# Kernel optimization log

Measured on AMD Instinct MI355X. Metric: run time of the kernel, lower is better.

Reference implementation:

```python
import jax, jax.numpy as jnp
import numpy as np

N_NODES = 100000
N_EDGES = 1600000
IN_F, HID_F, OUT_F = 64, 64, 16


def setup_inputs() -> dict:
    key = jax.random.key(0)
    k_x, k_e, k_w1, k_w2 = jax.random.split(key, 4)
    x = jax.random.normal(k_x, (N_NODES, IN_F), dtype=jnp.float32)
    edge_index = jax.random.randint(k_e, (2, N_EDGES), 0, N_NODES, dtype=jnp.int64)
    # Glorot-ish init for the GCNConv linear weights; bias zeros (PyG default)
    W1 = jax.random.normal(k_w1, (IN_F, HID_F), dtype=jnp.float32) / np.sqrt(IN_F)
    b1 = jnp.zeros((HID_F,), dtype=jnp.float32)
    W2 = jax.random.normal(k_w2, (HID_F, OUT_F), dtype=jnp.float32) / np.sqrt(HID_F)
    b2 = jnp.zeros((OUT_F,), dtype=jnp.float32)
    return {"x": x, "edge_index": edge_index, "W1": W1, "b1": b1, "W2": W2, "b2": b2}


def reference(x, edge_index, W1, b1, W2, b2):
    N = x.shape[0]
    # GCNConv: add self-loops, symmetric normalization D^-1/2 A D^-1/2
    loop = jnp.arange(N, dtype=edge_index.dtype)
    src = jnp.concatenate([edge_index[0], loop])  # [E+N]
    dst = jnp.concatenate([edge_index[1], loop])  # [E+N]
    deg = jax.ops.segment_sum(jnp.ones_like(dst, dtype=x.dtype), dst, num_segments=N)
    dis = jax.lax.rsqrt(deg)  # deg >= 1 due to self-loops
    norm = dis[src] * dis[dst]  # [E+N]

    def gcn_conv(h, W, b):
        h = h @ W                                   # [N, d_out]
        msg = h[src] * norm[:, None]                # gather + scale  [E+N, d_out]
        agg = jax.ops.segment_sum(msg, dst, num_segments=N)  # scatter-add
        return agg + b

    h = jax.nn.relu(gcn_conv(x, W1, b1))
    h = gcn_conv(h, W2, b2)
    return jax.nn.log_softmax(h, axis=1)
```

## Files before the change

kernel.cpp:

```cpp
#include <hip/hip_runtime.h>
#include <hip/hip_bf16.h>
#include <hip/hip_fp16.h>


#define F1 64
#define F2 16
#define NBKT 256
#define BSH 512
#define NSB 256
#define SBD 1024
#define STG 9216

typedef _Float16 f16x8 __attribute__((ext_vector_type(8)));
typedef _Float16 f16x4 __attribute__((ext_vector_type(4)));
typedef float f32x2 __attribute__((ext_vector_type(2)));
typedef float f32x4 __attribute__((ext_vector_type(4)));
typedef float f32x8 __attribute__((ext_vector_type(8)));

__device__ inline f32x8 shfl_xor_f32x8(f32x8 v, int off) {
  f32x8 r;
#pragma unroll
  for (int k = 0; k < 8; ++k) r[k] = __shfl_xor(v[k], off);
  return r;
}
__device__ inline f32x4 shfl_xor_f32x4(f32x4 v, int off) {
  f32x4 r;
#pragma unroll
  for (int k = 0; k < 4; ++k) r[k] = __shfl_xor(v[k], off);
  return r;
}

__device__ inline void acc_fp8x8(f32x8& a, uint2 v) {
  f32x2 p0 = __builtin_amdgcn_cvt_pk_f32_fp8((int)v.x, false);
  f32x2 p1 = __builtin_amdgcn_cvt_pk_f32_fp8((int)v.x, true);
  f32x2 p2 = __builtin_amdgcn_cvt_pk_f32_fp8((int)v.y, false);
  f32x2 p3 = __builtin_amdgcn_cvt_pk_f32_fp8((int)v.y, true);
  a[0] += p0[0]; a[1] += p0[1]; a[2] += p1[0]; a[3] += p1[1];
  a[4] += p2[0]; a[5] += p2[1]; a[6] += p3[0]; a[7] += p3[1];
}

__global__ void k_scatterL(const int* __restrict__ src, const int* __restrict__ dst,
                           int* __restrict__ tmp, int* __restrict__ segstart,
                           int E, int nb, int chunk,
                           const float* __restrict__ W1, const float* __restrict__ W2,
                           const float* __restrict__ b1,
                           __half* __restrict__ W1T, __half* __restrict__ W2Tp,
                           float* __restrict__ b1p) {
  int t = threadIdx.x, sb = blockIdx.x;
  if (sb == NSB) {
    for (int i = t; i < 64 * 64; i += SBD) {
      int n = i >> 6, k = i & 63;
      W1T[i] = __float2half(W1[k * 64 + n]);
    }
    for (int i = t; i < 16 * 64; i += SBD) {
      int j = i >> 6, p = i & 63;
      int fp = 16 * (p & 3) + (p >> 2);
      W2Tp[i] = __float2half(W2[fp * 16 + j]);
    }
    if (t < 64) b1p[t] = b1[16 * (t & 3) + (t >> 2)];
    return;
  }
  __shared__ int h[NBKT];
  __shared__ int cur[NBKT];
  __shared__ int sc[NBKT];
  int beg = sb * chunk, end = min(beg + chunk, E);
  for (int i = t; i < NBKT; i += SBD) h[i] = 0;
  __syncthreads();
  int e;
  for (e = beg + t * 4; e + 4 <= end; e += 4 * SBD) {
    int4 d4 = *(const int4*)(dst + e);
    atomicAdd(&h[d4.x >> 9], 1);
    atomicAdd(&h[d4.y >> 9], 1);
    atomicAdd(&h[d4.z >> 9], 1);
    atomicAdd(&h[d4.w >> 9], 1);
  }
  for (; e < end; ++e) atomicAdd(&h[dst[e] >> 9], 1);
  __syncthreads();
  if (t < NBKT) sc[t] = h[t];
  __syncthreads();
  for (int off = 1; off < NBKT; off <<= 1) {
    int a = (t < NBKT && t >= off) ? sc[t - off] : 0;
    __syncthreads();
    if (t < NBKT) sc[t] += a;
    __syncthreads();
  }
  if (t < NBKT) cur[t] = (t == 0) ? 0 : sc[t - 1];
  __syncthreads();
  for (int i = t; i < nb; i += SBD) segstart[sb * (nb + 1) + i] = beg + cur[i];
  if (t == 0) segstart[sb * (nb + 1) + nb] = end;
  __syncthreads();
  for (e = beg + t * 4; e + 4 <= end; e += 4 * SBD) {
    int4 d4 = *(const int4*)(dst + e);
    int4 s4 = *(const int4*)(src + e);
    int b, off;
    b = d4.x >> 9; off = atomicAdd(&cur[b], 1); tmp[beg + off] = (s4.x << 9) | (d4.x & 511);
    b = d4.y >> 9; off = atomicAdd(&cur[b], 1); tmp[beg + off] = (s4.y << 9) | (d4.y & 511);
    b = d4.z >> 9; off = atomicAdd(&cur[b], 1); tmp[beg + off] = (s4.z << 9) | (d4.z & 511);
    b = d4.w >> 9; off = atomicAdd(&cur[b], 1); tmp[beg + off] = (s4.w << 9) | (d4.w & 511);
  }
  for (; e < end; ++e) {
    int d = dst[e];
    int b = d >> 9;
    int off = atomicAdd(&cur[b], 1);
    tmp[beg + off] = (src[e] << 9) | (d & 511);
  }
}

__global__ void k_csr(const int* __restrict__ tmp, const int* __restrict__ segstart,
                      int* __restrict__ csr, int* __restrict__ rowptr,
                      float* __restrict__ dis, int N, int nb, int chunk) {
  __shared__ int stage[STG];
  __shared__ int sc[BSH];
  __shared__ int cnt[BSH];
  __shared__ int lofs[BSH];
  __shared__ int s_beg;
  int b = blockIdx.x, t = threadIdx.x;
  int s0 = 0, len = 0;
  if (t < NSB) {
    s0 = segstart[t * (nb + 1) + b];
    len = segstart[t * (nb + 1) + b + 1] - s0;
  }
  sc[t] = (t < NSB) ? (s0 - t * chunk) : 0;
  __syncthreads();
  for (int off = BSH / 2; off > 0; off >>= 1) {
    if (t < off) sc[t] += sc[t + off];
    __syncthreads();
  }
  if (t == 0) s_beg = sc[0];
  __syncthreads();
  int beg = s_beg;
  sc[t] = (t < NSB) ? len : 0;
  __syncthreads();
  for (int off = 1; off < NSB; off <<= 1) {
    int a = (t < NSB && t >= off) ? sc[t - off] : 0;
    __syncthreads();
    if (t < NSB) sc[t] += a;
    __syncthreads();
  }
  int total = sc[NSB - 1];
  int my0 = (t == 0) ? 0 : ((t < NSB) ? sc[t - 1] : 0);
  if (t < NSB) {
    int i = 0;
    for (; i + 4 <= len; i += 4) {
      int v0 = tmp[s0 + i], v1 = tmp[s0 + i + 1], v2 = tmp[s0 + i + 2], v3 = tmp[s0 + i + 3];
      stage[my0 + i] = v0; stage[my0 + i + 1] = v1;
      stage[my0 + i + 2] = v2; stage[my0 + i + 3] = v3;
    }
    for (; i < len; ++i) stage[my0 + i] = tmp[s0 + i];
  }
  cnt[t] = 0;
  __syncthreads();
  for (int i = t; i < total; i += BSH) atomicAdd(&cnt[stage[i] & (BSH - 1)], 1);
  __syncthreads();
  sc[t] = cnt[t];
  __syncthreads();
  for (int off = 1; off < BSH; off <<= 1) {
    int a = (t >= off) ? sc[t - off] : 0;
    __syncthreads();
    sc[t] += a;
    __syncthreads();
  }
  int excl = (t == 0) ? 0 : sc[t - 1];
  lofs[t] = excl;
  int n = b * BSH + t;
  if (n <= N) rowptr[n] = beg + excl;
  if (n < N) dis[n] = rsqrtf((float)(cnt[t] + 1));
  cnt[t] = 0;
  __syncthreads();
  for (int i = t; i < total; i += BSH) {
    int p = stage[i];
    int l = p & (BSH - 1);
    int off = atomicAdd(&cnt[l], 1);
    csr[beg + lofs[l] + off] = p >> 9;
  }
}

__global__ void k_gemm1(const float* __restrict__ x, const __half* __restrict__ W1T,
                        const float* __restrict__ dis, unsigned char* __restrict__ out,
                        int N) {
  int t = threadIdx.x;
  int wv = t >> 6, lane = t & 63;
  int m = lane & 15, q = lane >> 4;
  int row0 = blockIdx.x * 64 + wv * 16;
  int arow = min(row0 + m, N - 1);
  const _Float16* wt = (const _Float16*)W1T;
  f16x8 bf[4][2];
#pragma unroll
  for (int c = 0; c < 4; ++c)
#pragma unroll
    for (int kt = 0; kt < 2; ++kt)
      bf[c][kt] = *(const f16x8*)&wt[(c * 16 + m) * 64 + kt * 32 + q * 8];
  f16x8 a[2];
#pragma unroll
  for (int kt = 0; kt < 2; ++kt) {
    const float4* xp = (const float4*)(x + (size_t)arow * 64 + kt * 32 + q * 8);
    float4 u = xp[0], v = xp[1];
    a[kt][0] = (_Float16)u.x; a[kt][1] = (_Float16)u.y;
    a[kt][2] = (_Float16)u.z; a[kt][3] = (_Float16)u.w;
    a[kt][4] = (_Float16)v.x; a[kt][5] = (_Float16)v.y;
    a[kt][6] = (_Float16)v.z; a[kt][7] = (_Float16)v.w;
  }
  f32x4 acc[4] = {};
#pragma unroll
  for (int kt = 0; kt < 2; ++kt)
#pragma unroll
    for (int c = 0; c < 4; ++c)
      acc[c] = __builtin_amdgcn_mfma_f32_16x16x32_f16(a[kt], bf[c][kt], acc[c], 0, 0, 0);
#pragma unroll
  for (int r = 0; r < 4; ++r) {
    int n = row0 + q * 4 + r;
    if (n < N) {
      float dn = dis[n];
      int d = __builtin_amdgcn_cvt_pk_fp8_f32(acc[0][r] * dn, acc[1][r] * dn, 0, false);
      d = __builtin_amdgcn_cvt_pk_fp8_f32(acc[2][r] * dn, acc[3][r] * dn, d, true);
      *(unsigned int*)(out + (size_t)n * 64 + m * 4) = (unsigned)d;
    }
  }
}

__global__ void k_agg1f(const unsigned char* __restrict__ h, const float* __restrict__ dis,
                        const int* __restrict__ rowptr, const int* __restrict__ csr,
                        const float* __restrict__ b1p, const __half* __restrict__ W2Tp,
                        __half* __restrict__ h2, int N) {
  int gt = blockIdx.x * blockDim.x + threadIdx.x;
  int w = gt >> 6;
  int lane = gt & 63;
  int half = lane >> 5;
  int sub = (lane >> 3) & 3;
  int fl = lane & 7;
  int n = w * 2 + half;
  if (n >= N) return;
  float dn = dis[n];
  float4 bu = *(const float4*)(b1p + fl * 8);
  float4 bv = *(const float4*)(b1p + fl * 8 + 4);
  const _Float16* wt = (const _Float16*)W2Tp;
  f16x8 wj[4];
#pragma unroll
  for (int i = 0; i < 4; ++i)
    wj[i] = *(const f16x8*)&wt[(sub * 4 + i) * 64 + fl * 8];
  f32x8 acc0 = {}, acc1 = {};
  if (sub == 0)
    acc_fp8x8(acc0, *(const uint2*)&h[(size_t)n * 64 + fl * 8]);
  int beg = rowptr[n], end = rowptr[n + 1];
  int e = beg + sub;
  int sA = (e < end) ? csr[e] : -1;
  int sB = (e + 4 < end) ? csr[e + 4] : -1;
  while (sB >= 0) {
    int e2 = e + 8;
    int sC = (e2 < end) ? csr[e2] : -1;
    int sD = (e2 + 4 < end) ? csr[e2 + 4] : -1;
    uint2 v0 = *(const uint2*)&h[(size_t)sA * 64 + fl * 8];
    uint2 v1 = *(const uint2*)&h[(size_t)sB * 64 + fl * 8];
    acc_fp8x8(acc0, v0);
    acc_fp8x8(acc1, v1);
    sA = sC; sB = sD; e = e2;
  }
  if (sA >= 0)
    acc_fp8x8(acc0, *(const uint2*)&h[(size_t)sA * 64 + fl * 8]);
  f32x8 acc = acc0 + acc1;
  acc += shfl_xor_f32x8(acc, 8);
  acc += shfl_xor_f32x8(acc, 16);
  float bb[8] = {bu.x, bu.y, bu.z, bu.w, bv.x, bv.y, bv.z, bv.w};
  float hr[8];
#pragma unroll
  for (int k = 0; k < 8; ++k)
    hr[k] = fmaxf(fmaf(dn, acc[k], bb[k]), 0.f);
  float p[4];
#pragma unroll
  for (int i = 0; i < 4; ++i) {
    float s = 0.f;
#pragma unroll
    for (int k = 0; k < 8; ++k) s = fmaf(hr[k], (float)wj[i][k], s);
    s += __shfl_xor(s, 1);
    s += __shfl_xor(s, 2);
    s += __shfl_xor(s, 4);
    p[i] = s;
  }
  if (fl == 0) {
    f16x4 o;
#pragma unroll
    for (int i = 0; i < 4; ++i) o[i] = (_Float16)(p[i] * dn);
    *(f16x4*)((_Float16*)h2 + (size_t)n * 16 + sub * 4) = o;
  }
}

__global__ void k_agg2(const __half* __restrict__ h2, const float* __restrict__ dis,
                       const int* __restrict__ rowptr, const int* __restrict__ csr,
                       const float* __restrict__ b2, float* __restrict__ out, int N) {
  int gt = blockIdx.x * blockDim.x + threadIdx.x;
  int w = gt >> 6;
  int lane = gt & 63;
  int half = lane >> 5;
  int sub = (lane >> 2) & 7;
  int fl = lane & 3;
  int n = w * 2 + half;
  if (n >= N) return;
  const _Float16* hp = (const _Float16*)h2;
  f32x4 acc0 = {}, acc1 = {};
  if (sub == 0)
    acc0 = __builtin_convertvector(*(const f16x4*)&hp[(size_t)n * 16 + fl * 4], f32x4);
  int beg = rowptr[n], end = rowptr[n + 1];
  int e = beg + sub;
  int sA = (e < end) ? csr[e] : -1;
  int sB = (e + 8 < end) ? csr[e + 8] : -1;
  while (sB >= 0) {
    int e2 = e + 16;
    int sC = (e2 < end) ? csr[e2] : -1;
    int sD = (e2 + 8 < end) ? csr[e2 + 8] : -1;
    f16x4 v0 = *(const f16x4*)&hp[(size_t)sA * 16 + fl * 4];
    f16x4 v1 = *(const f16x4*)&hp[(size_t)sB * 16 + fl * 4];
    acc0 += __builtin_convertvector(v0, f32x4);
    acc1 += __builtin_convertvector(v1, f32x4);
    sA = sC; sB = sD; e = e2;
  }
  if (sA >= 0)
    acc0 += __builtin_convertvector(*(const f16x4*)&hp[(size_t)sA * 16 + fl * 4], f32x4);
  f32x4 acc = acc0 + acc1;
  acc += shfl_xor_f32x4(acc, 4);
  acc += shfl_xor_f32x4(acc, 8);
  acc += shfl_xor_f32x4(acc, 16);
  if (sub == 0) {
    float dn = dis[n];
    float4 bb = *(const float4*)(b2 + fl * 4);
    float v0 = fmaf(dn, acc[0], bb.x);
    float v1 = fmaf(dn, acc[1], bb.y);
    float v2 = fmaf(dn, acc[2], bb.z);
    float v3 = fmaf(dn, acc[3], bb.w);
    float m = fmaxf(fmaxf(v0, v1), fmaxf(v2, v3));
    m = fmaxf(m, __shfl_xor(m, 1));
    m = fmaxf(m, __shfl_xor(m, 2));
    float s2 = __expf(v0 - m) + __expf(v1 - m) + __expf(v2 - m) + __expf(v3 - m);
    s2 += __shfl_xor(s2, 1);
    s2 += __shfl_xor(s2, 2);
    float ls = m + __logf(s2);
    float4 o = {v0 - ls, v1 - ls, v2 - ls, v3 - ls};
    *(float4*)(out + (size_t)n * 16 + fl * 4) = o;
  }
}

extern "C" void kernel_launch(void* const* d_in, const int* in_sizes, int n_in,
                              void* d_out, int out_size, void* d_ws, size_t ws_size,
                              hipStream_t stream) {
  const float* x = (const float*)d_in[0];
  const int* ei = (const int*)d_in[1];
  const float* W1 = (const float*)d_in[2];
  const float* b1 = (const float*)d_in[3];
  const float* W2 = (const float*)d_in[4];
  const float* b2 = (const float*)d_in[5];
  float* out = (float*)d_out;

  int N = in_sizes[0] / F1;
  int E = in_sizes[1] / 2;
  const int* src = ei;
  const int* dst = ei + E;
  int nb = (N + BSH - 1) >> 9;
  int chunk = ((E + NSB - 1) / NSB + 3) & ~3;

  char* ws = (char*)d_ws;
  size_t o_w1t = 0;
  size_t o_w2t = o_w1t + 64 * 64 * 2;
  size_t o_b1p = (o_w2t + 16 * 64 * 2 + 255) & ~(size_t)255;
  size_t o_seg = (o_b1p + 64 * 4 + 255) & ~(size_t)255;
  size_t o_dis = (o_seg + (size_t)NSB * (nb + 1) * 4 + 255) & ~(size_t)255;
  size_t o_rowp = (o_dis + (size_t)N * 4 + 255) & ~(size_t)255;
  size_t o_tmp = (o_rowp + (size_t)(N + 1) * 4 + 255) & ~(size_t)255;
  size_t o_csr = (o_tmp + (size_t)NSB * chunk * 4 + 255) & ~(size_t)255;
  size_t o_h1 = (o_csr + (size_t)E * 4 + 255) & ~(size_t)255;
  size_t o_h2 = (o_h1 + (size_t)N * 64 + 255) & ~(size_t)255;

  __half* W1T = (__half*)(ws + o_w1t);
  __half* W2Tp = (__half*)(ws + o_w2t);
  float* b1p = (float*)(ws + o_b1p);
  int* segst = (int*)(ws + o_seg);
  float* dis = (float*)(ws + o_dis);
  int* rowptr = (int*)(ws + o_rowp);
  int* tmp = (int*)(ws + o_tmp);
  int* csr = (int*)(ws + o_csr);
  unsigned char* h1 = (unsigned char*)(ws + o_h1);
  __half* h2 = (__half*)(ws + o_h2);

  k_scatterL<<<NSB + 1, SBD, 0, stream>>>(src, dst, tmp, segst, E, nb, chunk,
                                          W1, W2, b1, W1T, W2Tp, b1p);
  k_csr<<<nb, BSH, 0, stream>>>(tmp, segst, csr, rowptr, dis, N, nb, chunk);

  int gb = (N + 63) / 64;
  k_gemm1<<<gb, 256, 0, stream>>>(x, W1T, dis, h1, N);
  int aw = (N + 1) / 2;
  k_agg1f<<<((size_t)aw * 64 + 255) / 256, 256, 0, stream>>>(h1, dis, rowptr, csr, b1p, W2Tp, h2, N);
  k_agg2<<<((size_t)aw * 64 + 255) / 256, 256, 0, stream>>>(h2, dis, rowptr, csr, b2, out, N);
}
```

Before: 181.1 us.

## Replace two-pass bucketed CSR build with global-atomic degree count and fill

Replaces the shared-memory bucket sort (per-block histogram, segment offsets, and a per-bucket staging/counting-sort kernel) with a global atomic degree histogram, a wave-scan allocation of row segments through an atomic counter, and an atomic-cursor fill of the CSR. Rows are no longer contiguous in node order, so the aggregation kernels read separate begin/end arrays. The intent is fewer passes and less shared-memory staging, at the cost of many scattered global atomics and a less local CSR write pattern. The fp8 accumulator is also reshaped into f32x2 pieces.

```diff
diff --git a/kernel.cpp b/kernel.cpp
--- a/kernel.cpp
+++ b/kernel.cpp
@@ -5,11 +5,8 @@
 
 #define F1 64
 #define F2 16
-#define NBKT 256
-#define BSH 512
-#define NSB 256
+#define NPB 256
 #define SBD 1024
-#define STG 9216
 
 typedef _Float16 f16x8 __attribute__((ext_vector_type(8)));
 typedef _Float16 f16x4 __attribute__((ext_vector_type(4)));
@@ -30,24 +27,20 @@
   return r;
 }
 
-__device__ inline void acc_fp8x8(f32x8& a, uint2 v) {
-  f32x2 p0 = __builtin_amdgcn_cvt_pk_f32_fp8((int)v.x, false);
-  f32x2 p1 = __builtin_amdgcn_cvt_pk_f32_fp8((int)v.x, true);
-  f32x2 p2 = __builtin_amdgcn_cvt_pk_f32_fp8((int)v.y, false);
-  f32x2 p3 = __builtin_amdgcn_cvt_pk_f32_fp8((int)v.y, true);
-  a[0] += p0[0]; a[1] += p0[1]; a[2] += p1[0]; a[3] += p1[1];
-  a[4] += p2[0]; a[5] += p2[1]; a[6] += p3[0]; a[7] += p3[1];
-}
-
-__global__ void k_scatterL(const int* __restrict__ src, const int* __restrict__ dst,
-                           int* __restrict__ tmp, int* __restrict__ segstart,
-                           int E, int nb, int chunk,
-                           const float* __restrict__ W1, const float* __restrict__ W2,
-                           const float* __restrict__ b1,
-                           __half* __restrict__ W1T, __half* __restrict__ W2Tp,
-                           float* __restrict__ b1p) {
+__device__ inline void acc_fp8x8(f32x2* a, uint2 v) {
+  a[0] += __builtin_amdgcn_cvt_pk_f32_fp8((int)v.x, false);
+  a[1] += __builtin_amdgcn_cvt_pk_f32_fp8((int)v.x, true);
+  a[2] += __builtin_amdgcn_cvt_pk_f32_fp8((int)v.y, false);
+  a[3] += __builtin_amdgcn_cvt_pk_f32_fp8((int)v.y, true);
+}
+
+__global__ void k_pre(const int* __restrict__ dst, int* __restrict__ deg, int E,
+                      const float* __restrict__ W1, const float* __restrict__ W2,
+                      const float* __restrict__ b1,
+                      __half* __restrict__ W1T, __half* __restrict__ W2Tp,
+                      float* __restrict__ b1p) {
   int t = threadIdx.x, sb = blockIdx.x;
-  if (sb == NSB) {
+  if (sb == NPB) {
     for (int i = t; i < 64 * 64; i += SBD) {
       int n = i >> 6, k = i & 63;
       W1T[i] = __float2half(W1[k * 64 + n]);
@@ -60,118 +53,65 @@
     if (t < 64) b1p[t] = b1[16 * (t & 3) + (t >> 2)];
     return;
   }
-  __shared__ int h[NBKT];
-  __shared__ int cur[NBKT];
-  __shared__ int sc[NBKT];
-  int beg = sb * chunk, end = min(beg + chunk, E);
-  for (int i = t; i < NBKT; i += SBD) h[i] = 0;
-  __syncthreads();
-  int e;
-  for (e = beg + t * 4; e + 4 <= end; e += 4 * SBD) {
-    int4 d4 = *(const int4*)(dst + e);
-    atomicAdd(&h[d4.x >> 9], 1);
-    atomicAdd(&h[d4.y >> 9], 1);
-    atomicAdd(&h[d4.z >> 9], 1);
-    atomicAdd(&h[d4.w >> 9], 1);
-  }
-  for (; e < end; ++e) atomicAdd(&h[dst[e] >> 9], 1);
-  __syncthreads();
-  if (t < NBKT) sc[t] = h[t];
-  __syncthreads();
-  for (int off = 1; off < NBKT; off <<= 1) {
-    int a = (t < NBKT && t >= off) ? sc[t - off] : 0;
-    __syncthreads();
-    if (t < NBKT) sc[t] += a;
-    __syncthreads();
-  }
-  if (t < NBKT) cur[t] = (t == 0) ? 0 : sc[t - 1];
-  __syncthreads();
-  for (int i = t; i < nb; i += SBD) segstart[sb * (nb + 1) + i] = beg + cur[i];
-  if (t == 0) segstart[sb * (nb + 1) + nb] = end;
-  __syncthreads();
-  for (e = beg + t * 4; e + 4 <= end; e += 4 * SBD) {
-    int4 d4 = *(const int4*)(dst + e);
-    int4 s4 = *(const int4*)(src + e);
-    int b, off;
-    b = d4.x >> 9; off = atomicAdd(&cur[b], 1); tmp[beg + off] = (s4.x << 9) | (d4.x & 511);
-    b = d4.y >> 9; off = atomicAdd(&cur[b], 1); tmp[beg + off] = (s4.y << 9) | (d4.y & 511);
-    b = d4.z >> 9; off = atomicAdd(&cur[b], 1); tmp[beg + off] = (s4.z << 9) | (d4.z & 511);
-    b = d4.w >> 9; off = atomicAdd(&cur[b], 1); tmp[beg + off] = (s4.w << 9) | (d4.w & 511);
-  }
-  for (; e < end; ++e) {
-    int d = dst[e];
-    int b = d >> 9;
-    int off = atomicAdd(&cur[b], 1);
-    tmp[beg + off] = (src[e] << 9) | (d & 511);
-  }
-}
-
-__global__ void k_csr(const int* __restrict__ tmp, const int* __restrict__ segstart,
-                      int* __restrict__ csr, int* __restrict__ rowptr,
-                      float* __restrict__ dis, int N, int nb, int chunk) {
-  __shared__ int stage[STG];
-  __shared__ int sc[BSH];
-  __shared__ int cnt[BSH];
-  __shared__ int lofs[BSH];
-  __shared__ int s_beg;
-  int b = blockIdx.x, t = threadIdx.x;
-  int s0 = 0, len = 0;
-  if (t < NSB) {
-    s0 = segstart[t * (nb + 1) + b];
-    len = segstart[t * (nb + 1) + b + 1] - s0;
-  }
-  sc[t] = (t < NSB) ? (s0 - t * chunk) : 0;
-  __syncthreads();
-  for (int off = BSH / 2; off > 0; off >>= 1) {
-    if (t < off) sc[t] += sc[t + off];
-    __syncthreads();
-  }
-  if (t == 0) s_beg = sc[0];
-  __syncthreads();
-  int beg = s_beg;
-  sc[t] = (t < NSB) ? len : 0;
-  __syncthreads();
-  for (int off = 1; off < NSB; off <<= 1) {
-    int a = (t < NSB && t >= off) ? sc[t - off] : 0;
-    __syncthreads();
-    if (t < NSB) sc[t] += a;
-    __syncthreads();
-  }
-  int total = sc[NSB - 1];
-  int my0 = (t == 0) ? 0 : ((t < NSB) ? sc[t - 1] : 0);
-  if (t < NSB) {
-    int i = 0;
-    for (; i + 4 <= len; i += 4) {
-      int v0 = tmp[s0 + i], v1 = tmp[s0 + i + 1], v2 = tmp[s0 + i + 2], v3 = tmp[s0 + i + 3];
-      stage[my0 + i] = v0; stage[my0 + i + 1] = v1;
-      stage[my0 + i + 2] = v2; stage[my0 + i + 3] = v3;
-    }
-    for (; i < len; ++i) stage[my0 + i] = tmp[s0 + i];
-  }
-  cnt[t] = 0;
-  __syncthreads();
-  for (int i = t; i < total; i += BSH) atomicAdd(&cnt[stage[i] & (BSH - 1)], 1);
-  __syncthreads();
-  sc[t] = cnt[t];
-  __syncthreads();
-  for (int off = 1; off < BSH; off <<= 1) {
-    int a = (t >= off) ? sc[t - off] : 0;
-    __syncthreads();
-    sc[t] += a;
-    __syncthreads();
-  }
-  int excl = (t == 0) ? 0 : sc[t - 1];
-  lofs[t] = excl;
-  int n = b * BSH + t;
-  if (n <= N) rowptr[n] = beg + excl;
-  if (n < N) dis[n] = rsqrtf((float)(cnt[t] + 1));
-  cnt[t] = 0;
-  __syncthreads();
-  for (int i = t; i < total; i += BSH) {
-    int p = stage[i];
-    int l = p & (BSH - 1);
-    int off = atomicAdd(&cnt[l], 1);
-    csr[beg + lofs[l] + off] = p >> 9;
+  int e4 = E >> 2;
+  int stride = NPB * SBD;
+  const int4* d4p = (const int4*)dst;
+  for (int i = sb * SBD + t; i < e4; i += stride) {
+    int4 d4 = d4p[i];
+    atomicAdd(&deg[d4.x], 1);
+    atomicAdd(&deg[d4.y], 1);
+    atomicAdd(&deg[d4.z], 1);
+    atomicAdd(&deg[d4.w], 1);
+  }
+  int tid = sb * SBD + t;
+  if (tid < (E & 3)) atomicAdd(&deg[dst[(E & ~3) + tid]], 1);
+}
+
+__global__ void k_alloc(const int* __restrict__ deg, int* __restrict__ ctr,
+                        int* __restrict__ rowbeg, int* __restrict__ rowcur,
+                        float* __restrict__ dis, int N) {
+  int n = blockIdx.x * blockDim.x + threadIdx.x;
+  int lane = threadIdx.x & 63;
+  int d = (n < N) ? deg[n] : 0;
+  int v = d;
+#pragma unroll
+  for (int off = 1; off < 64; off <<= 1) {
+    int u = __shfl_up(v, off);
+    if (lane >= off) v += u;
+  }
+  int tot = __shfl(v, 63);
+  int wbase = 0;
+  if (lane == 0) wbase = atomicAdd(ctr, tot);
+  wbase = __shfl(wbase, 0);
+  if (n < N) {
+    int b0 = wbase + v - d;
+    rowbeg[n] = b0;
+    rowcur[n] = b0;
+    dis[n] = rsqrtf((float)(d + 1));
+  }
+}
+
+__global__ void k_fill(const int* __restrict__ src, const int* __restrict__ dst,
+                       int* __restrict__ rowcur, int* __restrict__ csr, int E) {
+  int t = threadIdx.x, sb = blockIdx.x;
+  int e4 = E >> 2;
+  int stride = NPB * SBD;
+  const int4* d4p = (const int4*)dst;
+  const int4* s4p = (const int4*)src;
+  for (int i = sb * SBD + t; i < e4; i += stride) {
+    int4 d4 = d4p[i];
+    int4 s4 = s4p[i];
+    int o;
+    o = atomicAdd(&rowcur[d4.x], 1); csr[o] = s4.x;
+    o = atomicAdd(&rowcur[d4.y], 1); csr[o] = s4.y;
+    o = atomicAdd(&rowcur[d4.z], 1); csr[o] = s4.z;
+    o = atomicAdd(&rowcur[d4.w], 1); csr[o] = s4.w;
+  }
+  int tid = sb * SBD + t;
+  if (tid < (E & 3)) {
+    int e = (E & ~3) + tid;
+    int o = atomicAdd(&rowcur[dst[e]], 1);
+    csr[o] = src[e];
   }
 }
 
@@ -219,7 +159,8 @@
 }
 
 __global__ void k_agg1f(const unsigned char* __restrict__ h, const float* __restrict__ dis,
-                        const int* __restrict__ rowptr, const int* __restrict__ csr,
+                        const int* __restrict__ rowbeg, const int* __restrict__ rowcur,
+                        const int* __restrict__ csr,
                         const float* __restrict__ b1p, const __half* __restrict__ W2Tp,
                         __half* __restrict__ h2, int N) {
   int gt = blockIdx.x * blockDim.x + threadIdx.x;
@@ -238,10 +179,10 @@
 #pragma unroll
   for (int i = 0; i < 4; ++i)
     wj[i] = *(const f16x8*)&wt[(sub * 4 + i) * 64 + fl * 8];
-  f32x8 acc0 = {}, acc1 = {};
+  f32x2 a0[4] = {}, a1[4] = {};
   if (sub == 0)
-    acc_fp8x8(acc0, *(const uint2*)&h[(size_t)n * 64 + fl * 8]);
-  int beg = rowptr[n], end = rowptr[n + 1];
+    acc_fp8x8(a0, *(const uint2*)&h[(size_t)n * 64 + fl * 8]);
+  int beg = rowbeg[n], end = rowcur[n];
   int e = beg + sub;
   int sA = (e < end) ? csr[e] : -1;
   int sB = (e + 4 < end) ? csr[e + 4] : -1;
@@ -251,13 +192,19 @@
     int sD = (e2 + 4 < end) ? csr[e2 + 4] : -1;
     uint2 v0 = *(const uint2*)&h[(size_t)sA * 64 + fl * 8];
     uint2 v1 = *(const uint2*)&h[(size_t)sB * 64 + fl * 8];
-    acc_fp8x8(acc0, v0);
-    acc_fp8x8(acc1, v1);
+    acc_fp8x8(a0, v0);
+    acc_fp8x8(a1, v1);
     sA = sC; sB = sD; e = e2;
   }
   if (sA >= 0)
-    acc_fp8x8(acc0, *(const uint2*)&h[(size_t)sA * 64 + fl * 8]);
-  f32x8 acc = acc0 + acc1;
+    acc_fp8x8(a0, *(const uint2*)&h[(size_t)sA * 64 + fl * 8]);
+  f32x8 acc;
+#pragma unroll
+  for (int k = 0; k < 4; ++k) {
+    f32x2 s = a0[k] + a1[k];
+    acc[2 * k] = s[0];
+    acc[2 * k + 1] = s[1];
+  }
   acc += shfl_xor_f32x8(acc, 8);
   acc += shfl_xor_f32x8(acc, 16);
   float bb[8] = {bu.x, bu.y, bu.z, bu.w, bv.x, bv.y, bv.z, bv.w};
@@ -285,7 +232,8 @@
 }
 
 __global__ void k_agg2(const __half* __restrict__ h2, const float* __restrict__ dis,
-                       const int* __restrict__ rowptr, const int* __restrict__ csr,
+                       const int* __restrict__ rowbeg, const int* __restrict__ rowcur,
+                       const int* __restrict__ csr,
                        const float* __restrict__ b2, float* __restrict__ out, int N) {
   int gt = blockIdx.x * blockDim.x + threadIdx.x;
   int w = gt >> 6;
@@ -299,7 +247,7 @@
   f32x4 acc0 = {}, acc1 = {};
   if (sub == 0)
     acc0 = __builtin_convertvector(*(const f16x4*)&hp[(size_t)n * 16 + fl * 4], f32x4);
-  int beg = rowptr[n], end = rowptr[n + 1];
+  int beg = rowbeg[n], end = rowcur[n];
   int e = beg + sub;
   int sA = (e < end) ? csr[e] : -1;
   int sB = (e + 8 < end) ? csr[e + 8] : -1;
@@ -353,39 +301,38 @@
   int E = in_sizes[1] / 2;
   const int* src = ei;
   const int* dst = ei + E;
-  int nb = (N + BSH - 1) >> 9;
-  int chunk = ((E + NSB - 1) / NSB + 3) & ~3;
 
   char* ws = (char*)d_ws;
   size_t o_w1t = 0;
   size_t o_w2t = o_w1t + 64 * 64 * 2;
   size_t o_b1p = (o_w2t + 16 * 64 * 2 + 255) & ~(size_t)255;
-  size_t o_seg = (o_b1p + 64 * 4 + 255) & ~(size_t)255;
-  size_t o_dis = (o_seg + (size_t)NSB * (nb + 1) * 4 + 255) & ~(size_t)255;
-  size_t o_rowp = (o_dis + (size_t)N * 4 + 255) & ~(size_t)255;
-  size_t o_tmp = (o_rowp + (size_t)(N + 1) * 4 + 255) & ~(size_t)255;
-  size_t o_csr = (o_tmp + (size_t)NSB * chunk * 4 + 255) & ~(size_t)255;
-  size_t o_h1 = (o_csr + (size_t)E * 4 + 255) & ~(size_t)255;
-  size_t o_h2 = (o_h1 + (size_t)N * 64 + 255) & ~(size_t)255;
+  size_t o_deg = (o_b1p + 64 * 4 + 255) & ~(size_t)255;
+  size_t o_rbg = (o_deg + (size_t)(N + 64) * 4 + 255) & ~(size_t)255;
+  size_t o_rcu = (o_rbg + (size_t)N * 4 + 255) & ~(size_t)255;
+  size_t o_dis = (o_rcu + (size_t)N * 4 + 255) & ~(size_t)255;
+  size_t o_csr = (o_dis + (size_t)N * 4 + 255) & ~(size_t)255;
+  size_t o_h1  = (o_csr + (size_t)E * 4 + 255) & ~(size_t)255;
+  size_t o_h2  = (o_h1 + (size_t)N * 64 + 255) & ~(size_t)255;
 
   __half* W1T = (__half*)(ws + o_w1t);
   __half* W2Tp = (__half*)(ws + o_w2t);
   float* b1p = (float*)(ws + o_b1p);
-  int* segst = (int*)(ws + o_seg);
+  int* deg = (int*)(ws + o_deg);
+  int* ctr = deg + N;
+  int* rowbeg = (int*)(ws + o_rbg);
+  int* rowcur = (int*)(ws + o_rcu);
   float* dis = (float*)(ws + o_dis);
-  int* rowptr = (int*)(ws + o_rowp);
-  int* tmp = (int*)(ws + o_tmp);
   int* csr = (int*)(ws + o_csr);
   unsigned char* h1 = (unsigned char*)(ws + o_h1);
   __half* h2 = (__half*)(ws + o_h2);
 
-  k_scatterL<<<NSB + 1, SBD, 0, stream>>>(src, dst, tmp, segst, E, nb, chunk,
-                                          W1, W2, b1, W1T, W2Tp, b1p);
-  k_csr<<<nb, BSH, 0, stream>>>(tmp, segst, csr, rowptr, dis, N, nb, chunk);
-
+  hipMemsetAsync(deg, 0, (size_t)(N + 64) * 4, stream);
+  k_pre<<<NPB + 1, SBD, 0, stream>>>(dst, deg, E, W1, W2, b1, W1T, W2Tp, b1p);
+  k_alloc<<<(N + 255) / 256, 256, 0, stream>>>(deg, ctr, rowbeg, rowcur, dis, N);
+  k_fill<<<NPB, SBD, 0, stream>>>(src, dst, rowcur, csr, E);
   int gb = (N + 63) / 64;
   k_gemm1<<<gb, 256, 0, stream>>>(x, W1T, dis, h1, N);
   int aw = (N + 1) / 2;
-  k_agg1f<<<((size_t)aw * 64 + 255) / 256, 256, 0, stream>>>(h1, dis, rowptr, csr, b1p, W2Tp, h2, N);
-  k_agg2<<<((size_t)aw * 64 + 255) / 256, 256, 0, stream>>>(h2, dis, rowptr, csr, b2, out, N);
-}
+  k_agg1f<<<((size_t)aw * 64 + 255) / 256, 256, 0, stream>>>(h1, dis, rowbeg, rowcur, csr, b1p, W2Tp, h2, N);
+  k_agg2<<<((size_t)aw * 64 + 255) / 256, 256, 0, stream>>>(h2, dis, rowbeg, rowcur, csr, b2, out, N);
+}
```

Measured after the change: 329.4 us. 82.0% more time.

## Fuse layer-1 GEMM into edge scatter kernel by moving source normalization to aggregation

Applied to the files above, without the earlier changes.

The layer-1 GEMM no longer scales its output by dis[n], so it no longer depends on the degree computation. Its blocks now run inside the edge bucketing kernel as extra blocks and overlap with the scatter. The source-side dis factor is applied in the layer-1 aggregation with a per-edge dis gather and packed FMAs. The weight preparation moves to a separate single-block kernel, and the scatter stage is reshaped to 512 blocks of 256 threads. The cost is an extra random dis load per edge in aggregation, plus fp8 quantization of unscaled values, which changes rounding.

```diff
diff --git a/kernel.cpp b/kernel.cpp
--- a/kernel.cpp
+++ b/kernel.cpp
@@ -7,8 +7,8 @@
 #define F2 16
 #define NBKT 256
 #define BSH 512
-#define NSB 256
-#define SBD 1024
+#define NSB 512
+#define SBD 256
 #define STG 9216
 
 typedef _Float16 f16x8 __attribute__((ext_vector_type(8)));
@@ -30,41 +30,82 @@
   return r;
 }
 
-__device__ inline void acc_fp8x8(f32x8& a, uint2 v) {
-  f32x2 p0 = __builtin_amdgcn_cvt_pk_f32_fp8((int)v.x, false);
-  f32x2 p1 = __builtin_amdgcn_cvt_pk_f32_fp8((int)v.x, true);
-  f32x2 p2 = __builtin_amdgcn_cvt_pk_f32_fp8((int)v.y, false);
-  f32x2 p3 = __builtin_amdgcn_cvt_pk_f32_fp8((int)v.y, true);
-  a[0] += p0[0]; a[1] += p0[1]; a[2] += p1[0]; a[3] += p1[1];
-  a[4] += p2[0]; a[5] += p2[1]; a[6] += p3[0]; a[7] += p3[1];
-}
-
-__global__ void k_scatterL(const int* __restrict__ src, const int* __restrict__ dst,
-                           int* __restrict__ tmp, int* __restrict__ segstart,
-                           int E, int nb, int chunk,
-                           const float* __restrict__ W1, const float* __restrict__ W2,
-                           const float* __restrict__ b1,
-                           __half* __restrict__ W1T, __half* __restrict__ W2Tp,
-                           float* __restrict__ b1p) {
+__device__ inline void fma_fp8x8(f32x2* a, uint2 v, float s) {
+  f32x2 sv = {s, s};
+  a[0] += sv * __builtin_amdgcn_cvt_pk_f32_fp8((int)v.x, false);
+  a[1] += sv * __builtin_amdgcn_cvt_pk_f32_fp8((int)v.x, true);
+  a[2] += sv * __builtin_amdgcn_cvt_pk_f32_fp8((int)v.y, false);
+  a[3] += sv * __builtin_amdgcn_cvt_pk_f32_fp8((int)v.y, true);
+}
+
+__global__ void k_w(const float* __restrict__ W1, const float* __restrict__ W2,
+                    const float* __restrict__ b1,
+                    __half* __restrict__ W1T, __half* __restrict__ W2Tp,
+                    float* __restrict__ b1p) {
+  int t = threadIdx.x;
+  for (int i = t; i < 64 * 64; i += 256) {
+    int n = i >> 6, k = i & 63;
+    W1T[i] = __float2half(W1[k * 64 + n]);
+  }
+  for (int i = t; i < 16 * 64; i += 256) {
+    int j = i >> 6, p = i & 63;
+    int fp = 16 * (p & 3) + (p >> 2);
+    W2Tp[i] = __float2half(W2[fp * 16 + j]);
+  }
+  if (t < 64) b1p[t] = b1[16 * (t & 3) + (t >> 2)];
+}
+
+__global__ void k_sg(const int* __restrict__ src, const int* __restrict__ dst,
+                     int* __restrict__ tmp, int* __restrict__ segstart,
+                     int E, int nb, int chunk,
+                     const float* __restrict__ x, const __half* __restrict__ W1T,
+                     unsigned char* __restrict__ h1, int N) {
   int t = threadIdx.x, sb = blockIdx.x;
-  if (sb == NSB) {
-    for (int i = t; i < 64 * 64; i += SBD) {
-      int n = i >> 6, k = i & 63;
-      W1T[i] = __float2half(W1[k * 64 + n]);
+  if (sb >= NSB) {
+    int g = sb - NSB;
+    int wv = t >> 6, lane = t & 63;
+    int m = lane & 15, q = lane >> 4;
+    int row0 = g * 64 + wv * 16;
+    int arow = min(row0 + m, N - 1);
+    const _Float16* wt = (const _Float16*)W1T;
+    f16x8 bf[4][2];
+#pragma unroll
+    for (int c = 0; c < 4; ++c)
+#pragma unroll
+      for (int kt = 0; kt < 2; ++kt)
+        bf[c][kt] = *(const f16x8*)&wt[(c * 16 + m) * 64 + kt * 32 + q * 8];
+    f16x8 a[2];
+#pragma unroll
+    for (int kt = 0; kt < 2; ++kt) {
+      const float4* xp = (const float4*)(x + (size_t)arow * 64 + kt * 32 + q * 8);
+      float4 u = xp[0], v = xp[1];
+      a[kt][0] = (_Float16)u.x; a[kt][1] = (_Float16)u.y;
+      a[kt][2] = (_Float16)u.z; a[kt][3] = (_Float16)u.w;
+      a[kt][4] = (_Float16)v.x; a[kt][5] = (_Float16)v.y;
+      a[kt][6] = (_Float16)v.z; a[kt][7] = (_Float16)v.w;
     }
-    for (int i = t; i < 16 * 64; i += SBD) {
-      int j = i >> 6, p = i & 63;
-      int fp = 16 * (p & 3) + (p >> 2);
-      W2Tp[i] = __float2half(W2[fp * 16 + j]);
+    f32x4 acc[4] = {};
+#pragma unroll
+    for (int kt = 0; kt < 2; ++kt)
+#pragma unroll
+      for (int c = 0; c < 4; ++c)
+        acc[c] = __builtin_amdgcn_mfma_f32_16x16x32_f16(a[kt], bf[c][kt], acc[c], 0, 0, 0);
+#pragma unroll
+    for (int r = 0; r < 4; ++r) {
+      int n = row0 + q * 4 + r;
+      if (n < N) {
+        int d = __builtin_amdgcn_cvt_pk_fp8_f32(acc[0][r], acc[1][r], 0, false);
+        d = __builtin_amdgcn_cvt_pk_fp8_f32(acc[2][r], acc[3][r], d, true);
+        *(unsigned int*)(h1 + (size_t)n * 64 + m * 4) = (unsigned)d;
+      }
     }
-    if (t < 64) b1p[t] = b1[16 * (t & 3) + (t >> 2)];
     return;
   }
   __shared__ int h[NBKT];
   __shared__ int cur[NBKT];
   __shared__ int sc[NBKT];
   int beg = sb * chunk, end = min(beg + chunk, E);
-  for (int i = t; i < NBKT; i += SBD) h[i] = 0;
+  h[t] = 0;
   __syncthreads();
   int e;
   for (e = beg + t * 4; e + 4 <= end; e += 4 * SBD) {
@@ -76,17 +117,17 @@
   }
   for (; e < end; ++e) atomicAdd(&h[dst[e] >> 9], 1);
   __syncthreads();
-  if (t < NBKT) sc[t] = h[t];
+  sc[t] = h[t];
   __syncthreads();
   for (int off = 1; off < NBKT; off <<= 1) {
-    int a = (t < NBKT && t >= off) ? sc[t - off] : 0;
-    __syncthreads();
-    if (t < NBKT) sc[t] += a;
-    __syncthreads();
-  }
-  if (t < NBKT) cur[t] = (t == 0) ? 0 : sc[t - 1];
-  __syncthreads();
-  for (int i = t; i < nb; i += SBD) segstart[sb * (nb + 1) + i] = beg + cur[i];
+    int a = (t >= off) ? sc[t - off] : 0;
+    __syncthreads();
+    sc[t] += a;
+    __syncthreads();
+  }
+  cur[t] = (t == 0) ? 0 : sc[t - 1];
+  __syncthreads();
+  if (t < nb) segstart[sb * (nb + 1) + t] = beg + cur[t];
   if (t == 0) segstart[sb * (nb + 1) + nb] = end;
   __syncthreads();
   for (e = beg + t * 4; e + 4 <= end; e += 4 * SBD) {
@@ -115,12 +156,9 @@
   __shared__ int lofs[BSH];
   __shared__ int s_beg;
   int b = blockIdx.x, t = threadIdx.x;
-  int s0 = 0, len = 0;
-  if (t < NSB) {
-    s0 = segstart[t * (nb + 1) + b];
-    len = segstart[t * (nb + 1) + b + 1] - s0;
-  }
-  sc[t] = (t < NSB) ? (s0 - t * chunk) : 0;
+  int s0 = segstart[t * (nb + 1) + b];
+  int len = segstart[t * (nb + 1) + b + 1] - s0;
+  sc[t] = s0 - t * chunk;
   __syncthreads();
   for (int off = BSH / 2; off > 0; off >>= 1) {
     if (t < off) sc[t] += sc[t + off];
@@ -129,17 +167,17 @@
   if (t == 0) s_beg = sc[0];
   __syncthreads();
   int beg = s_beg;
-  sc[t] = (t < NSB) ? len : 0;
+  sc[t] = len;
   __syncthreads();
   for (int off = 1; off < NSB; off <<= 1) {
-    int a = (t < NSB && t >= off) ? sc[t - off] : 0;
-    __syncthreads();
-    if (t < NSB) sc[t] += a;
+    int a = (t >= off) ? sc[t - off] : 0;
+    __syncthreads();
+    sc[t] += a;
     __syncthreads();
   }
   int total = sc[NSB - 1];
-  int my0 = (t == 0) ? 0 : ((t < NSB) ? sc[t - 1] : 0);
-  if (t < NSB) {
+  int my0 = (t == 0) ? 0 : sc[t - 1];
+  {
     int i = 0;
     for (; i + 4 <= len; i += 4) {
       int v0 = tmp[s0 + i], v1 = tmp[s0 + i + 1], v2 = tmp[s0 + i + 2], v3 = tmp[s0 + i + 3];
@@ -172,49 +210,6 @@
     int l = p & (BSH - 1);
     int off = atomicAdd(&cnt[l], 1);
     csr[beg + lofs[l] + off] = p >> 9;
-  }
-}
-
-__global__ void k_gemm1(const float* __restrict__ x, const __half* __restrict__ W1T,
-                        const float* __restrict__ dis, unsigned char* __restrict__ out,
-                        int N) {
-  int t = threadIdx.x;
-  int wv = t >> 6, lane = t & 63;
-  int m = lane & 15, q = lane >> 4;
-  int row0 = blockIdx.x * 64 + wv * 16;
-  int arow = min(row0 + m, N - 1);
-  const _Float16* wt = (const _Float16*)W1T;
-  f16x8 bf[4][2];
-#pragma unroll
-  for (int c = 0; c < 4; ++c)
-#pragma unroll
-    for (int kt = 0; kt < 2; ++kt)
-      bf[c][kt] = *(const f16x8*)&wt[(c * 16 + m) * 64 + kt * 32 + q * 8];
-  f16x8 a[2];
-#pragma unroll
-  for (int kt = 0; kt < 2; ++kt) {
-    const float4* xp = (const float4*)(x + (size_t)arow * 64 + kt * 32 + q * 8);
-    float4 u = xp[0], v = xp[1];
-    a[kt][0] = (_Float16)u.x; a[kt][1] = (_Float16)u.y;
-    a[kt][2] = (_Float16)u.z; a[kt][3] = (_Float16)u.w;
-    a[kt][4] = (_Float16)v.x; a[kt][5] = (_Float16)v.y;
-    a[kt][6] = (_Float16)v.z; a[kt][7] = (_Float16)v.w;
-  }
-  f32x4 acc[4] = {};
-#pragma unroll
-  for (int kt = 0; kt < 2; ++kt)
-#pragma unroll
-    for (int c = 0; c < 4; ++c)
-      acc[c] = __builtin_amdgcn_mfma_f32_16x16x32_f16(a[kt], bf[c][kt], acc[c], 0, 0, 0);
-#pragma unroll
-  for (int r = 0; r < 4; ++r) {
-    int n = row0 + q * 4 + r;
-    if (n < N) {
-      float dn = dis[n];
-      int d = __builtin_amdgcn_cvt_pk_fp8_f32(acc[0][r] * dn, acc[1][r] * dn, 0, false);
-      d = __builtin_amdgcn_cvt_pk_fp8_f32(acc[2][r] * dn, acc[3][r] * dn, d, true);
-      *(unsigned int*)(out + (size_t)n * 64 + m * 4) = (unsigned)d;
-    }
   }
 }
 
@@ -238,26 +233,36 @@
 #pragma unroll
   for (int i = 0; i < 4; ++i)
     wj[i] = *(const f16x8*)&wt[(sub * 4 + i) * 64 + fl * 8];
-  f32x8 acc0 = {}, acc1 = {};
+  f32x2 a0[4] = {}, a1[4] = {};
   if (sub == 0)
-    acc_fp8x8(acc0, *(const uint2*)&h[(size_t)n * 64 + fl * 8]);
+    fma_fp8x8(a0, *(const uint2*)&h[(size_t)n * 64 + fl * 8], dn);
   int beg = rowptr[n], end = rowptr[n + 1];
   int e = beg + sub;
   int sA = (e < end) ? csr[e] : -1;
   int sB = (e + 4 < end) ? csr[e + 4] : -1;
+  float dA = (sA >= 0) ? dis[sA] : 0.f;
+  float dB = (sB >= 0) ? dis[sB] : 0.f;
   while (sB >= 0) {
     int e2 = e + 8;
     int sC = (e2 < end) ? csr[e2] : -1;
     int sD = (e2 + 4 < end) ? csr[e2 + 4] : -1;
+    float dC = (sC >= 0) ? dis[sC] : 0.f;
+    float dD = (sD >= 0) ? dis[sD] : 0.f;
     uint2 v0 = *(const uint2*)&h[(size_t)sA * 64 + fl * 8];
     uint2 v1 = *(const uint2*)&h[(size_t)sB * 64 + fl * 8];
-    acc_fp8x8(acc0, v0);
-    acc_fp8x8(acc1, v1);
-    sA = sC; sB = sD; e = e2;
+    fma_fp8x8(a0, v0, dA);
+    fma_fp8x8(a1, v1, dB);
+    sA = sC; sB = sD; dA = dC; dB = dD; e = e2;
   }
   if (sA >= 0)
-    acc_fp8x8(acc0, *(const uint2*)&h[(size_t)sA * 64 + fl * 8]);
-  f32x8 acc = acc0 + acc1;
+    fma_fp8x8(a0, *(const uint2*)&h[(size_t)sA * 64 + fl * 8], dA);
+  f32x8 acc;
+#pragma unroll
+  for (int k = 0; k < 4; ++k) {
+    f32x2 s = a0[k] + a1[k];
+    acc[2 * k] = s[0];
+    acc[2 * k + 1] = s[1];
+  }
   acc += shfl_xor_f32x8(acc, 8);
   acc += shfl_xor_f32x8(acc, 16);
   float bb[8] = {bu.x, bu.y, bu.z, bu.w, bv.x, bv.y, bv.z, bv.w};
@@ -379,12 +384,11 @@
   unsigned char* h1 = (unsigned char*)(ws + o_h1);
   __half* h2 = (__half*)(ws + o_h2);
 
-  k_scatterL<<<NSB + 1, SBD, 0, stream>>>(src, dst, tmp, segst, E, nb, chunk,
-                                          W1, W2, b1, W1T, W2Tp, b1p);
+  int gb = (N + 63) / 64;
+  k_w<<<1, 256, 0, stream>>>(W1, W2, b1, W1T, W2Tp, b1p);
+  k_sg<<<NSB + gb, SBD, 0, stream>>>(src, dst, tmp, segst, E, nb, chunk,
+                                     x, W1T, h1, N);
   k_csr<<<nb, BSH, 0, stream>>>(tmp, segst, csr, rowptr, dis, N, nb, chunk);
-
-  int gb = (N + 63) / 64;
-  k_gemm1<<<gb, 256, 0, stream>>>(x, W1T, dis, h1, N);
   int aw = (N + 1) / 2;
   k_agg1f<<<((size_t)aw * 64 + 255) / 256, 256, 0, stream>>>(h1, dis, rowptr, csr, b1p, W2Tp, h2, N);
   k_agg2<<<((size_t)aw * 64 + 255) / 256, 256, 0, stream>>>(h2, dis, rowptr, csr, b2, out, N);
```

Measured after the change: 186.6 us. 3.1% more time.

## Bucket edges into fixed-capacity global slots via atomic cursors instead of segment tables

Applied to the files above, without the earlier changes.

The per-block segment-offset table is replaced by a global per-bucket cursor array. Each scatter block reserves space in fixed-capacity bucket slots (STG each) with one global atomic per bucket. The CSR kernel can then load its bucket as one contiguous span with int4 loads, instead of gathering 256 scattered segments and running extra scans. This adds a small setup kernel and assumes no bucket exceeds STG edges, which is risky for skewed degree distributions. The fp8 accumulate helper is also rewritten to use packed f32x2 adds.

```diff
diff --git a/kernel.cpp b/kernel.cpp
--- a/kernel.cpp
+++ b/kernel.cpp
@@ -7,7 +7,7 @@
 #define F2 16
 #define NBKT 256
 #define BSH 512
-#define NSB 256
+#define NPB 256
 #define SBD 1024
 #define STG 9216
 
@@ -30,41 +30,39 @@
   return r;
 }
 
-__device__ inline void acc_fp8x8(f32x8& a, uint2 v) {
-  f32x2 p0 = __builtin_amdgcn_cvt_pk_f32_fp8((int)v.x, false);
-  f32x2 p1 = __builtin_amdgcn_cvt_pk_f32_fp8((int)v.x, true);
-  f32x2 p2 = __builtin_amdgcn_cvt_pk_f32_fp8((int)v.y, false);
-  f32x2 p3 = __builtin_amdgcn_cvt_pk_f32_fp8((int)v.y, true);
-  a[0] += p0[0]; a[1] += p0[1]; a[2] += p1[0]; a[3] += p1[1];
-  a[4] += p2[0]; a[5] += p2[1]; a[6] += p3[0]; a[7] += p3[1];
-}
-
-__global__ void k_scatterL(const int* __restrict__ src, const int* __restrict__ dst,
-                           int* __restrict__ tmp, int* __restrict__ segstart,
-                           int E, int nb, int chunk,
-                           const float* __restrict__ W1, const float* __restrict__ W2,
-                           const float* __restrict__ b1,
-                           __half* __restrict__ W1T, __half* __restrict__ W2Tp,
-                           float* __restrict__ b1p) {
-  int t = threadIdx.x, sb = blockIdx.x;
-  if (sb == NSB) {
-    for (int i = t; i < 64 * 64; i += SBD) {
-      int n = i >> 6, k = i & 63;
-      W1T[i] = __float2half(W1[k * 64 + n]);
-    }
-    for (int i = t; i < 16 * 64; i += SBD) {
-      int j = i >> 6, p = i & 63;
-      int fp = 16 * (p & 3) + (p >> 2);
-      W2Tp[i] = __float2half(W2[fp * 16 + j]);
-    }
-    if (t < 64) b1p[t] = b1[16 * (t & 3) + (t >> 2)];
-    return;
-  }
+__device__ inline void acc_fp8x8(f32x2* a, uint2 v) {
+  a[0] += __builtin_amdgcn_cvt_pk_f32_fp8((int)v.x, false);
+  a[1] += __builtin_amdgcn_cvt_pk_f32_fp8((int)v.x, true);
+  a[2] += __builtin_amdgcn_cvt_pk_f32_fp8((int)v.y, false);
+  a[3] += __builtin_amdgcn_cvt_pk_f32_fp8((int)v.y, true);
+}
+
+__global__ void k_w(const float* __restrict__ W1, const float* __restrict__ W2,
+                    const float* __restrict__ b1,
+                    __half* __restrict__ W1T, __half* __restrict__ W2Tp,
+                    float* __restrict__ b1p, int* __restrict__ bcur, int nb) {
+  int t = threadIdx.x;
+  for (int i = t; i < 64 * 64; i += 256) {
+    int n = i >> 6, k = i & 63;
+    W1T[i] = __float2half(W1[k * 64 + n]);
+  }
+  for (int i = t; i < 16 * 64; i += 256) {
+    int j = i >> 6, p = i & 63;
+    int fp = 16 * (p & 3) + (p >> 2);
+    W2Tp[i] = __float2half(W2[fp * 16 + j]);
+  }
+  if (t < 64) b1p[t] = b1[16 * (t & 3) + (t >> 2)];
+  if (t < nb) bcur[t] = t * STG;
+}
+
+__global__ void k_bscatter(const int* __restrict__ src, const int* __restrict__ dst,
+                           int* __restrict__ bcur, int* __restrict__ tmp,
+                           int E, int nb, int chunk) {
   __shared__ int h[NBKT];
   __shared__ int cur[NBKT];
-  __shared__ int sc[NBKT];
+  int t = threadIdx.x, sb = blockIdx.x;
   int beg = sb * chunk, end = min(beg + chunk, E);
-  for (int i = t; i < NBKT; i += SBD) h[i] = 0;
+  if (t < NBKT) h[t] = 0;
   __syncthreads();
   int e;
   for (e = beg + t * 4; e + 4 <= end; e += 4 * SBD) {
@@ -76,7 +74,35 @@
   }
   for (; e < end; ++e) atomicAdd(&h[dst[e] >> 9], 1);
   __syncthreads();
-  if (t < NBKT) sc[t] = h[t];
+  if (t < nb) cur[t] = atomicAdd(&bcur[t], h[t]);
+  __syncthreads();
+  for (e = beg + t * 4; e + 4 <= end; e += 4 * SBD) {
+    int4 d4 = *(const int4*)(dst + e);
+    int4 s4 = *(const int4*)(src + e);
+    int b, off;
+    b = d4.x >> 9; off = atomicAdd(&cur[b], 1); tmp[off] = (s4.x << 9) | (d4.x & 511);
+    b = d4.y >> 9; off = atomicAdd(&cur[b], 1); tmp[off] = (s4.y << 9) | (d4.y & 511);
+    b = d4.z >> 9; off = atomicAdd(&cur[b], 1); tmp[off] = (s4.z << 9) | (d4.z & 511);
+    b = d4.w >> 9; off = atomicAdd(&cur[b], 1); tmp[off] = (s4.w << 9) | (d4.w & 511);
+  }
+  for (; e < end; ++e) {
+    int d = dst[e];
+    int b = d >> 9;
+    int off = atomicAdd(&cur[b], 1);
+    tmp[off] = (src[e] << 9) | (d & 511);
+  }
+}
+
+__global__ void k_csr(const int* __restrict__ tmp, const int* __restrict__ bcur,
+                      int* __restrict__ csr, int* __restrict__ rowptr,
+                      float* __restrict__ dis, int N, int nb) {
+  __shared__ int stage[STG];
+  __shared__ int sc[BSH];
+  __shared__ int cnt[BSH];
+  __shared__ int lofs[BSH];
+  int b = blockIdx.x, t = threadIdx.x;
+  int lenb = bcur[b] - b * STG;
+  if (t < NBKT) sc[t] = (t < nb) ? (bcur[t] - t * STG) : 0;
   __syncthreads();
   for (int off = 1; off < NBKT; off <<= 1) {
     int a = (t < NBKT && t >= off) ? sc[t - off] : 0;
@@ -84,73 +110,19 @@
     if (t < NBKT) sc[t] += a;
     __syncthreads();
   }
-  if (t < NBKT) cur[t] = (t == 0) ? 0 : sc[t - 1];
-  __syncthreads();
-  for (int i = t; i < nb; i += SBD) segstart[sb * (nb + 1) + i] = beg + cur[i];
-  if (t == 0) segstart[sb * (nb + 1) + nb] = end;
-  __syncthreads();
-  for (e = beg + t * 4; e + 4 <= end; e += 4 * SBD) {
-    int4 d4 = *(const int4*)(dst + e);
-    int4 s4 = *(const int4*)(src + e);
-    int b, off;
-    b = d4.x >> 9; off = atomicAdd(&cur[b], 1); tmp[beg + off] = (s4.x << 9) | (d4.x & 511);
-    b = d4.y >> 9; off = atomicAdd(&cur[b], 1); tmp[beg + off] = (s4.y << 9) | (d4.y & 511);
-    b = d4.z >> 9; off = atomicAdd(&cur[b], 1); tmp[beg + off] = (s4.z << 9) | (d4.z & 511);
-    b = d4.w >> 9; off = atomicAdd(&cur[b], 1); tmp[beg + off] = (s4.w << 9) | (d4.w & 511);
-  }
-  for (; e < end; ++e) {
-    int d = dst[e];
-    int b = d >> 9;
-    int off = atomicAdd(&cur[b], 1);
-    tmp[beg + off] = (src[e] << 9) | (d & 511);
-  }
-}
-
-__global__ void k_csr(const int* __restrict__ tmp, const int* __restrict__ segstart,
-                      int* __restrict__ csr, int* __restrict__ rowptr,
-                      float* __restrict__ dis, int N, int nb, int chunk) {
-  __shared__ int stage[STG];
-  __shared__ int sc[BSH];
-  __shared__ int cnt[BSH];
-  __shared__ int lofs[BSH];
-  __shared__ int s_beg;
-  int b = blockIdx.x, t = threadIdx.x;
-  int s0 = 0, len = 0;
-  if (t < NSB) {
-    s0 = segstart[t * (nb + 1) + b];
-    len = segstart[t * (nb + 1) + b + 1] - s0;
-  }
-  sc[t] = (t < NSB) ? (s0 - t * chunk) : 0;
-  __syncthreads();
-  for (int off = BSH / 2; off > 0; off >>= 1) {
-    if (t < off) sc[t] += sc[t + off];
-    __syncthreads();
-  }
-  if (t == 0) s_beg = sc[0];
-  __syncthreads();
-  int beg = s_beg;
-  sc[t] = (t < NSB) ? len : 0;
-  __syncthreads();
-  for (int off = 1; off < NSB; off <<= 1) {
-    int a = (t < NSB && t >= off) ? sc[t - off] : 0;
-    __syncthreads();
-    if (t < NSB) sc[t] += a;
-    __syncthreads();
-  }
-  int total = sc[NSB - 1];
-  int my0 = (t == 0) ? 0 : ((t < NSB) ? sc[t - 1] : 0);
-  if (t < NSB) {
-    int i = 0;
-    for (; i + 4 <= len; i += 4) {
-      int v0 = tmp[s0 + i], v1 = tmp[s0 + i + 1], v2 = tmp[s0 + i + 2], v3 = tmp[s0 + i + 3];
-      stage[my0 + i] = v0; stage[my0 + i + 1] = v1;
-      stage[my0 + i + 2] = v2; stage[my0 + i + 3] = v3;
-    }
-    for (; i < len; ++i) stage[my0 + i] = tmp[s0 + i];
+  int beg = (b == 0) ? 0 : sc[b - 1];
+  __syncthreads();
+  int s0 = b * STG;
+  int lim = lenb & ~3;
+  for (int i = t * 4; i < lim; i += 4 * BSH)
+    *(int4*)(stage + i) = *(const int4*)(tmp + s0 + i);
+  {
+    int r = lim + t;
+    if (r < lenb) stage[r] = tmp[s0 + r];
   }
   cnt[t] = 0;
   __syncthreads();
-  for (int i = t; i < total; i += BSH) atomicAdd(&cnt[stage[i] & (BSH - 1)], 1);
+  for (int i = t; i < lenb; i += BSH) atomicAdd(&cnt[stage[i] & (BSH - 1)], 1);
   __syncthreads();
   sc[t] = cnt[t];
   __syncthreads();
@@ -167,7 +139,7 @@
   if (n < N) dis[n] = rsqrtf((float)(cnt[t] + 1));
   cnt[t] = 0;
   __syncthreads();
-  for (int i = t; i < total; i += BSH) {
+  for (int i = t; i < lenb; i += BSH) {
     int p = stage[i];
     int l = p & (BSH - 1);
     int off = atomicAdd(&cnt[l], 1);
@@ -238,9 +210,9 @@
 #pragma unroll
   for (int i = 0; i < 4; ++i)
     wj[i] = *(const f16x8*)&wt[(sub * 4 + i) * 64 + fl * 8];
-  f32x8 acc0 = {}, acc1 = {};
+  f32x2 a0[4] = {}, a1[4] = {};
   if (sub == 0)
-    acc_fp8x8(acc0, *(const uint2*)&h[(size_t)n * 64 + fl * 8]);
+    acc_fp8x8(a0, *(const uint2*)&h[(size_t)n * 64 + fl * 8]);
   int beg = rowptr[n], end = rowptr[n + 1];
   int e = beg + sub;
   int sA = (e < end) ? csr[e] : -1;
@@ -251,13 +223,19 @@
     int sD = (e2 + 4 < end) ? csr[e2 + 4] : -1;
     uint2 v0 = *(const uint2*)&h[(size_t)sA * 64 + fl * 8];
     uint2 v1 = *(const uint2*)&h[(size_t)sB * 64 + fl * 8];
-    acc_fp8x8(acc0, v0);
-    acc_fp8x8(acc1, v1);
+    acc_fp8x8(a0, v0);
+    acc_fp8x8(a1, v1);
     sA = sC; sB = sD; e = e2;
   }
   if (sA >= 0)
-    acc_fp8x8(acc0, *(const uint2*)&h[(size_t)sA * 64 + fl * 8]);
-  f32x8 acc = acc0 + acc1;
+    acc_fp8x8(a0, *(const uint2*)&h[(size_t)sA * 64 + fl * 8]);
+  f32x8 acc;
+#pragma unroll
+  for (int k = 0; k < 4; ++k) {
+    f32x2 s = a0[k] + a1[k];
+    acc[2 * k] = s[0];
+    acc[2 * k + 1] = s[1];
+  }
   acc += shfl_xor_f32x8(acc, 8);
   acc += shfl_xor_f32x8(acc, 16);
   float bb[8] = {bu.x, bu.y, bu.z, bu.w, bv.x, bv.y, bv.z, bv.w};
@@ -354,24 +332,24 @@
   const int* src = ei;
   const int* dst = ei + E;
   int nb = (N + BSH - 1) >> 9;
-  int chunk = ((E + NSB - 1) / NSB + 3) & ~3;
+  int chunk = ((E + NPB - 1) / NPB + 3) & ~3;
 
   char* ws = (char*)d_ws;
   size_t o_w1t = 0;
   size_t o_w2t = o_w1t + 64 * 64 * 2;
   size_t o_b1p = (o_w2t + 16 * 64 * 2 + 255) & ~(size_t)255;
-  size_t o_seg = (o_b1p + 64 * 4 + 255) & ~(size_t)255;
-  size_t o_dis = (o_seg + (size_t)NSB * (nb + 1) * 4 + 255) & ~(size_t)255;
+  size_t o_bcur = (o_b1p + 64 * 4 + 255) & ~(size_t)255;
+  size_t o_dis = (o_bcur + NBKT * 4 + 255) & ~(size_t)255;
   size_t o_rowp = (o_dis + (size_t)N * 4 + 255) & ~(size_t)255;
   size_t o_tmp = (o_rowp + (size_t)(N + 1) * 4 + 255) & ~(size_t)255;
-  size_t o_csr = (o_tmp + (size_t)NSB * chunk * 4 + 255) & ~(size_t)255;
+  size_t o_csr = (o_tmp + (size_t)nb * STG * 4 + 255) & ~(size_t)255;
   size_t o_h1 = (o_csr + (size_t)E * 4 + 255) & ~(size_t)255;
   size_t o_h2 = (o_h1 + (size_t)N * 64 + 255) & ~(size_t)255;
 
   __half* W1T = (__half*)(ws + o_w1t);
   __half* W2Tp = (__half*)(ws + o_w2t);
   float* b1p = (float*)(ws + o_b1p);
-  int* segst = (int*)(ws + o_seg);
+  int* bcur = (int*)(ws + o_bcur);
   float* dis = (float*)(ws + o_dis);
   int* rowptr = (int*)(ws + o_rowp);
   int* tmp = (int*)(ws + o_tmp);
@@ -379,10 +357,9 @@
   unsigned char* h1 = (unsigned char*)(ws + o_h1);
   __half* h2 = (__half*)(ws + o_h2);
 
-  k_scatterL<<<NSB + 1, SBD, 0, stream>>>(src, dst, tmp, segst, E, nb, chunk,
-                                          W1, W2, b1, W1T, W2Tp, b1p);
-  k_csr<<<nb, BSH, 0, stream>>>(tmp, segst, csr, rowptr, dis, N, nb, chunk);
-
+  k_w<<<1, 256, 0, stream>>>(W1, W2, b1, W1T, W2Tp, b1p, bcur, nb);
+  k_bscatter<<<NPB, SBD, 0, stream>>>(src, dst, bcur, tmp, E, nb, chunk);
+  k_csr<<<nb, BSH, 0, stream>>>(tmp, bcur, csr, rowptr, dis, N, nb);
   int gb = (N + 63) / 64;
   k_gemm1<<<gb, 256, 0, stream>>>(x, W1T, dis, h1, N);
   int aw = (N + 1) / 2;
```

Measured after the change: 184.3 us. No clear change (+1.8%).
